# Performance work log

Hardware: AMD Instinct MI355X
Metric: run time of the kernel (lower is better)

## Reference

```python
import jax, jax.numpy as jnp
import numpy as np


def _box_filter(img):
    # img: [B,1,H,W]; 5x5 uniform kernel, padding=4 -> output [B,1,H+4,W+4]
    k = jnp.full((1, 1, 5, 5), 1.0 / 25.0, dtype=img.dtype)
    return jax.lax.conv_general_dilated(
        img, k, window_strides=(1, 1), padding=((4, 4), (4, 4)),
        dimension_numbers=('NCHW', 'OIHW', 'NCHW'))


def setup_inputs() -> dict:
    key = jax.random.key(0)
    k1, k2 = jax.random.split(key)
    x = jax.random.normal(k1, (64, 1, 512, 512), dtype=jnp.float32)
    y = jax.random.normal(k2, (64, 1, 512, 512), dtype=jnp.float32)
    return {"x": x, "y": y}


def reference(x, y):
    diff = _box_filter(x) - _box_filter(y)
    # faithful to torch.mean(torch.sqrt(diff * diff)) (== mean(|diff|))
    return jnp.mean(jnp.sqrt(diff * diff))
```

## Files before the change

kernel.cpp:

```cpp
#include <hip/hip_runtime.h>


#define IMG_W 512
#define IMG_H 512
#define OUT_W 516
#define OUT_H 516
#define TR    16
#define NT    256

__global__ __launch_bounds__(NT) void box_loss_kernel(
    const float* __restrict__ x, const float* __restrict__ y,
    float* __restrict__ partial)
{
    __shared__ float ring[5][IMG_W];
    __shared__ float vbuf[2][OUT_W + 4];
    __shared__ float wsum[NT / 64];

    const int t  = threadIdx.x;
    const int b  = blockIdx.y;
    const int i0 = blockIdx.x * TR;
    const int c0 = 2 * t;

    const float* xb = x + (size_t)b * IMG_W * IMG_H;
    const float* yb = y + (size_t)b * IMG_W * IMG_H;

    #pragma unroll
    for (int s = 0; s < 5; ++s) {
        ring[s][c0] = 0.f; ring[s][c0 + 1] = 0.f;
    }
    if (t < 4) {
        vbuf[0][t] = 0.f;         vbuf[1][t] = 0.f;
        vbuf[0][OUT_W + t] = 0.f; vbuf[1][OUT_W + t] = 0.f;
    }

    float v0 = 0.f, v1 = 0.f;
    for (int r = i0 - 4; r < i0; ++r) {
        float d0 = 0.f, d1 = 0.f;
        if (r >= 0) {
            float2 xv = *(const float2*)(xb + (size_t)r * IMG_W + c0);
            float2 yv = *(const float2*)(yb + (size_t)r * IMG_W + c0);
            d0 = xv.x - yv.x; d1 = xv.y - yv.y;
        }
        int slot = (r + 5) % 5;
        ring[slot][c0] = d0; ring[slot][c0 + 1] = d1;
        v0 += d0; v1 += d1;
    }

    const int nrows = min(TR, OUT_H - i0);
    float acc = 0.f;
    int buf = 0;
    for (int ii = 0; ii < nrows; ++ii) {
        const int i = i0 + ii;
        float d0 = 0.f, d1 = 0.f;
        if (i < IMG_H) {
            float2 xv = *(const float2*)(xb + (size_t)i * IMG_W + c0);
            float2 yv = *(const float2*)(yb + (size_t)i * IMG_W + c0);
            d0 = xv.x - yv.x; d1 = xv.y - yv.y;
        }
        const int slot = i % 5;
        float o0 = ring[slot][c0], o1 = ring[slot][c0 + 1];
        v0 += d0 - o0; v1 += d1 - o1;
        ring[slot][c0] = d0; ring[slot][c0 + 1] = d1;

        vbuf[buf][4 + c0]     = v0;
        vbuf[buf][4 + c0 + 1] = v1;
        __syncthreads();

        const float* __restrict__ vb = vbuf[buf];
        float s0 = vb[t]     + vb[t + 1]   + vb[t + 2]   + vb[t + 3]   + vb[t + 4];
        float s1 = vb[t+256] + vb[t + 257] + vb[t + 258] + vb[t + 259] + vb[t + 260];
        acc += fabsf(s0) + fabsf(s1);
        if (t < 4) {
            float s2 = vb[t+512] + vb[t+513] + vb[t+514] + vb[t+515] + vb[t+516];
            acc += fabsf(s2);
        }
        buf ^= 1;
    }

    #pragma unroll
    for (int off = 32; off > 0; off >>= 1)
        acc += __shfl_down(acc, off, 64);
    if ((t & 63) == 0) wsum[t >> 6] = acc;
    __syncthreads();
    if (t == 0) {
        float s = wsum[0] + wsum[1] + wsum[2] + wsum[3];
        atomicAdd(partial, s);
    }
}

__global__ void finalize_kernel(const float* __restrict__ partial,
                                float* __restrict__ out)
{
    out[0] = partial[0] * (1.0f / (25.0f * 64.0f * 516.0f * 516.0f));
}

extern "C" void kernel_launch(void* const* d_in, const int* in_sizes, int n_in,
                              void* d_out, int out_size, void* d_ws, size_t ws_size,
                              hipStream_t stream) {
    const float* x = (const float*)d_in[0];
    const float* y = (const float*)d_in[1];
    float* out = (float*)d_out;
    float* ws  = (float*)d_ws;

    hipMemsetAsync(ws, 0, sizeof(float), stream);

    dim3 grid((OUT_H + TR - 1) / TR, 64);
    box_loss_kernel<<<grid, NT, 0, stream>>>(x, y, ws);
    finalize_kernel<<<1, 1, 0, stream>>>(ws, out);
}
```

Measured before the change: 171.1 us.

## Process row strips per wavefront with register ring and shuffle-based horizontal sums

Work is restructured so each 64-lane wavefront owns an 8-row strip of one image, and each lane covers 8 columns. The vertical running sums and the 5-row history ring move from shared memory into registers. The horizontal 5-wide window uses __shfl_up of neighbour sums instead of a shared buffer guarded by __syncthreads. This removes the per-row block barrier and the LDS traffic. The shorter strips mean more halo rows are reloaded per output row, about 12 rows read per 8 produced, and register pressure rises. Atomics are spread over 64 partial slots, which the finalize kernel then sums.

After: 170.4 us. No clear change (-0.4%).

```diff
diff --git a/kernel.cpp b/kernel.cpp
--- a/kernel.cpp
+++ b/kernel.cpp
@@ -5,93 +5,121 @@
 #define IMG_H 512
 #define OUT_W 516
 #define OUT_H 516
-#define TR    16
+#define R     8
+#define SPI   65
 #define NT    256
+#define WAVES (NT / 64)
+#define NSTRIPS (64 * SPI)
+#define NPART 64
 
 __global__ __launch_bounds__(NT) void box_loss_kernel(
     const float* __restrict__ x, const float* __restrict__ y,
     float* __restrict__ partial)
 {
-    __shared__ float ring[5][IMG_W];
-    __shared__ float vbuf[2][OUT_W + 4];
-    __shared__ float wsum[NT / 64];
+    const int t    = threadIdx.x;
+    const int lane = t & 63;
+    const int wid  = t >> 6;
+    const int strip = blockIdx.x * WAVES + wid;
+    const int b  = strip / SPI;
+    const int s  = strip - b * SPI;
+    const int i0 = s * R;
+    const int c0 = lane * 8;
 
-    const int t  = threadIdx.x;
-    const int b  = blockIdx.y;
-    const int i0 = blockIdx.x * TR;
-    const int c0 = 2 * t;
+    const float* xb = x + (size_t)b * (IMG_W * IMG_H) + c0;
+    const float* yb = y + (size_t)b * (IMG_W * IMG_H) + c0;
 
-    const float* xb = x + (size_t)b * IMG_W * IMG_H;
-    const float* yb = y + (size_t)b * IMG_W * IMG_H;
+    float ring[5][8];
+    float v[8];
+    #pragma unroll
+    for (int j = 0; j < 8; ++j) { v[j] = 0.f; ring[4][j] = 0.f; }
 
     #pragma unroll
-    for (int s = 0; s < 5; ++s) {
-        ring[s][c0] = 0.f; ring[s][c0 + 1] = 0.f;
-    }
-    if (t < 4) {
-        vbuf[0][t] = 0.f;         vbuf[1][t] = 0.f;
-        vbuf[0][OUT_W + t] = 0.f; vbuf[1][OUT_W + t] = 0.f;
+    for (int w = 0; w < 4; ++w) {
+        const int r = i0 - 4 + w;
+        float d[8] = {0.f, 0.f, 0.f, 0.f, 0.f, 0.f, 0.f, 0.f};
+        if (r >= 0) {
+            const float* xr = xb + (size_t)r * IMG_W;
+            const float* yr = yb + (size_t)r * IMG_W;
+            const float4 xa = *(const float4*)(xr);
+            const float4 xc = *(const float4*)(xr + 4);
+            const float4 ya = *(const float4*)(yr);
+            const float4 yc = *(const float4*)(yr + 4);
+            d[0] = xa.x - ya.x; d[1] = xa.y - ya.y;
+            d[2] = xa.z - ya.z; d[3] = xa.w - ya.w;
+            d[4] = xc.x - yc.x; d[5] = xc.y - yc.y;
+            d[6] = xc.z - yc.z; d[7] = xc.w - yc.w;
+        }
+        #pragma unroll
+        for (int j = 0; j < 8; ++j) { ring[w][j] = d[j]; v[j] += d[j]; }
     }
 
-    float v0 = 0.f, v1 = 0.f;
-    for (int r = i0 - 4; r < i0; ++r) {
-        float d0 = 0.f, d1 = 0.f;
-        if (r >= 0) {
-            float2 xv = *(const float2*)(xb + (size_t)r * IMG_W + c0);
-            float2 yv = *(const float2*)(yb + (size_t)r * IMG_W + c0);
-            d0 = xv.x - yv.x; d1 = xv.y - yv.y;
+    float acc = 0.f;
+
+    #pragma unroll
+    for (int ii = 0; ii < R; ++ii) {
+        const int i = i0 + ii;
+        if (i >= OUT_H) break;
+
+        float d[8] = {0.f, 0.f, 0.f, 0.f, 0.f, 0.f, 0.f, 0.f};
+        if (i < IMG_H) {
+            const float* xr = xb + (size_t)i * IMG_W;
+            const float* yr = yb + (size_t)i * IMG_W;
+            const float4 xa = *(const float4*)(xr);
+            const float4 xc = *(const float4*)(xr + 4);
+            const float4 ya = *(const float4*)(yr);
+            const float4 yc = *(const float4*)(yr + 4);
+            d[0] = xa.x - ya.x; d[1] = xa.y - ya.y;
+            d[2] = xa.z - ya.z; d[3] = xa.w - ya.w;
+            d[4] = xc.x - yc.x; d[5] = xc.y - yc.y;
+            d[6] = xc.z - yc.z; d[7] = xc.w - yc.w;
         }
-        int slot = (r + 5) % 5;
-        ring[slot][c0] = d0; ring[slot][c0 + 1] = d1;
-        v0 += d0; v1 += d1;
-    }
+        const int slot = (ii + 4) % 5;
+        #pragma unroll
+        for (int j = 0; j < 8; ++j) {
+            v[j] += d[j] - ring[slot][j];
+            ring[slot][j] = d[j];
+        }
 
-    const int nrows = min(TR, OUT_H - i0);
-    float acc = 0.f;
-    int buf = 0;
-    for (int ii = 0; ii < nrows; ++ii) {
-        const int i = i0 + ii;
-        float d0 = 0.f, d1 = 0.f;
-        if (i < IMG_H) {
-            float2 xv = *(const float2*)(xb + (size_t)i * IMG_W + c0);
-            float2 yv = *(const float2*)(yb + (size_t)i * IMG_W + c0);
-            d0 = xv.x - yv.x; d1 = xv.y - yv.y;
+        float h0 = __shfl_up(v[4], 1, 64);
+        float h1 = __shfl_up(v[5], 1, 64);
+        float h2 = __shfl_up(v[6], 1, 64);
+        float h3 = __shfl_up(v[7], 1, 64);
+        if (lane == 0) { h0 = 0.f; h1 = 0.f; h2 = 0.f; h3 = 0.f; }
+
+        const float s0 = h0 + h1 + h2 + h3 + v[0];
+        const float s1 = s0 + v[1] - h0;
+        const float s2 = s1 + v[2] - h1;
+        const float s3 = s2 + v[3] - h2;
+        const float s4 = s3 + v[4] - h3;
+        const float s5 = s4 + v[5] - v[0];
+        const float s6 = s5 + v[6] - v[1];
+        const float s7 = s6 + v[7] - v[2];
+        acc += fabsf(s0) + fabsf(s1) + fabsf(s2) + fabsf(s3)
+             + fabsf(s4) + fabsf(s5) + fabsf(s6) + fabsf(s7);
+
+        if (lane == 63) {
+            const float e0 = v[4] + v[5] + v[6] + v[7];
+            const float e1 = v[5] + v[6] + v[7];
+            const float e2 = v[6] + v[7];
+            const float e3 = v[7];
+            acc += fabsf(e0) + fabsf(e1) + fabsf(e2) + fabsf(e3);
         }
-        const int slot = i % 5;
-        float o0 = ring[slot][c0], o1 = ring[slot][c0 + 1];
-        v0 += d0 - o0; v1 += d1 - o1;
-        ring[slot][c0] = d0; ring[slot][c0 + 1] = d1;
-
-        vbuf[buf][4 + c0]     = v0;
-        vbuf[buf][4 + c0 + 1] = v1;
-        __syncthreads();
-
-        const float* __restrict__ vb = vbuf[buf];
-        float s0 = vb[t]     + vb[t + 1]   + vb[t + 2]   + vb[t + 3]   + vb[t + 4];
-        float s1 = vb[t+256] + vb[t + 257] + vb[t + 258] + vb[t + 259] + vb[t + 260];
-        acc += fabsf(s0) + fabsf(s1);
-        if (t < 4) {
-            float s2 = vb[t+512] + vb[t+513] + vb[t+514] + vb[t+515] + vb[t+516];
-            acc += fabsf(s2);
-        }
-        buf ^= 1;
     }
 
     #pragma unroll
     for (int off = 32; off > 0; off >>= 1)
         acc += __shfl_down(acc, off, 64);
-    if ((t & 63) == 0) wsum[t >> 6] = acc;
-    __syncthreads();
-    if (t == 0) {
-        float s = wsum[0] + wsum[1] + wsum[2] + wsum[3];
-        atomicAdd(partial, s);
-    }
+    if (lane == 0)
+        atomicAdd(partial + (strip & (NPART - 1)), acc);
 }
 
 __global__ void finalize_kernel(const float* __restrict__ partial,
                                 float* __restrict__ out)
 {
-    out[0] = partial[0] * (1.0f / (25.0f * 64.0f * 516.0f * 516.0f));
+    float s = 0.f;
+    #pragma unroll
+    for (int k = 0; k < NPART; ++k) s += partial[k];
+    out[0] = s * (1.0f / (25.0f * 64.0f * 516.0f * 516.0f));
 }
 
 extern "C" void kernel_launch(void* const* d_in, const int* in_sizes, int n_in,
@@ -102,9 +130,9 @@
     float* out = (float*)d_out;
     float* ws  = (float*)d_ws;
 
-    hipMemsetAsync(ws, 0, sizeof(float), stream);
+    hipMemsetAsync(ws, 0, NPART * sizeof(float), stream);
 
-    dim3 grid((OUT_H + TR - 1) / TR, 64);
+    dim3 grid(NSTRIPS / WAVES);
     box_loss_kernel<<<grid, NT, 0, stream>>>(x, y, ws);
     finalize_kernel<<<1, 1, 0, stream>>>(ws, out);
 }
```
